# Performance work log

Hardware: AMD Instinct MI355X
Metric: run time of the kernel (lower is better)

The kernel has to match this reference:

```python
import jax, jax.numpy as jnp
import numpy as np

NUM_CLASSES = 32
SIGMA = 0.02
LOG_SIGMA = float(np.log(SIGMA))
HALF_LOG_2PI = float(0.5 * np.log(2.0 * np.pi))


def _gcn(x, adj, W1, b1, W2, b2):
    # Two-layer GCN: h = relu(A x W1 + b1); out = A h W2 + b2
    h = jax.nn.relu(jnp.einsum('bij,bjf->bif', adj, x) @ W1 + b1)
    return jnp.einsum('bij,bjf->bif', adj, h) @ W2 + b2


def setup_inputs() -> dict:
    key = jax.random.key(0)
    ks = jax.random.split(key, 10)
    B, N, F = 64, 1024, 512
    x = jax.random.normal(ks[0], (B, N, F), dtype=jnp.float32)
    adj = jax.random.uniform(ks[1], (B, N, N), dtype=jnp.float32) / N  # row-scaled dense adjacency
    masks = jax.random.randint(ks[2], (B, N, F), 0, 2, dtype=jnp.int32)
    noise = jax.random.normal(ks[3], (B, N, F), dtype=jnp.float32)
    s = 0.05
    We1 = jax.random.normal(ks[4], (F, 30), dtype=jnp.float32) * s
    be1 = jnp.zeros((30,), dtype=jnp.float32)
    We2 = jax.random.normal(ks[5], (30, 18), dtype=jnp.float32) * s
    be2 = jnp.zeros((18,), dtype=jnp.float32)
    Wd1 = jax.random.normal(ks[6], (18, 30), dtype=jnp.float32) * s
    bd1 = jnp.zeros((30,), dtype=jnp.float32)
    Wd2 = jax.random.normal(ks[7], (30, F), dtype=jnp.float32) * s
    bd2 = jnp.zeros((F,), dtype=jnp.float32)
    return dict(x=x, adj=adj, masks=masks, noise=noise, We1=We1, be1=be1,
                We2=We2, be2=be2, Wd1=Wd1, bd1=bd1, Wd2=Wd2, bd2=bd2)


def reference(x, adj, masks, noise, We1, be1, We2, be2, Wd1, bd1, Wd2, bd2):
    enc = _gcn(x, adj, We1, be1, We2, be2)            # [B,N,18]
    dec = _gcn(enc, adj, Wd1, bd1, Wd2, bd2)          # [B,N,F]
    dec_act = jnp.concatenate(
        (jax.nn.softmax(dec[..., :NUM_CLASSES], axis=-1),
         jax.nn.sigmoid(dec[..., NUM_CLASSES:])), axis=-1)
    m = masks.astype(dec_act.dtype)
    # Vectorized masked reparameterized Gaussian sample: s = mu + sigma*eps
    sampled = dec_act + m * (SIGMA * noise)
    # log N(s; mu, sigma) = -eps^2/2 - log(sigma) - 0.5*log(2pi), summed over masked entries
    lp_elem = -0.5 * noise * noise - LOG_SIGMA - HALF_LOG_2PI
    log_probs = jnp.sum(m * lp_elem, axis=(1, 2))      # [B]
    return dec, sampled, log_probs
```

## Files before the change

kernel.cpp:

```cpp
#include <hip/hip_runtime.h>

#define B_ 64
#define NN 1024
#define FF 512

typedef float  fx4 __attribute__((ext_vector_type(4)));
typedef float  fx2 __attribute__((ext_vector_type(2)));
typedef int    ix4 __attribute__((ext_vector_type(4)));
typedef unsigned int   ux4i __attribute__((ext_vector_type(4)));
typedef unsigned int   ux2i __attribute__((ext_vector_type(2)));
typedef unsigned short us4  __attribute__((ext_vector_type(4)));
typedef short  sx8 __attribute__((ext_vector_type(8)));

#define FP8_SCALE   16384.0f
#define INV_SCALE   6.103515625e-5f

static __device__ __forceinline__ unsigned short f2bf(float f){
    union { float f; unsigned u; } v; v.f = f;
    unsigned r = v.u + 0x7FFFu + ((v.u >> 16) & 1u);
    return (unsigned short)(r >> 16);
}
static __device__ __forceinline__ float bf2f(unsigned short h){
    union { unsigned u; float f; } v; v.u = ((unsigned)h) << 16;
    return v.f;
}
static __device__ __forceinline__ unsigned cvt_pk_bf16(float lo, float hi){
    unsigned r;
    asm("v_cvt_pk_bf16_f32 %0, %1, %2" : "=v"(r) : "v"(lo), "v"(hi));
    return r;
}
static __device__ __forceinline__ sx8 pack_bf16x8(fx4 v0, fx4 v1){
    union { unsigned u[4]; sx8 s; } r;
    r.u[0] = cvt_pk_bf16(v0[0], v0[1]);
    r.u[1] = cvt_pk_bf16(v0[2], v0[3]);
    r.u[2] = cvt_pk_bf16(v1[0], v1[1]);
    r.u[3] = cvt_pk_bf16(v1[2], v1[3]);
    return r.s;
}

__global__ __launch_bounds__(512) void k_xw1(
    const float* __restrict__ x, const float* __restrict__ We1,
    unsigned short* __restrict__ u1T){
    __shared__ unsigned short wls[32*512];
    int tid = threadIdx.x;
    for (int i = tid; i < 32*512; i += 512){
        int col = i >> 9, k = i & 511;
        float v = (col < 30) ? We1[k*30 + col] : 0.f;
        wls[col*512 + ((((k >> 3) ^ (col & 7)) << 3) | (k & 7))] = f2bf(v);
    }
    __syncthreads();
    int w = tid >> 6, l = tid & 63;
    int lr = l & 15, kq = l >> 4;
    int b = blockIdx.y;
    int rowb = blockIdx.x*128 + w*16;
    const float* xp = x + ((size_t)b*NN + rowb + lr)*FF + kq*8;
    fx4 acc0 = {0,0,0,0}, acc1 = {0,0,0,0};
    int c0 = lr, c1 = 16 + lr;
    #pragma unroll 4
    for (int kk = 0; kk < FF; kk += 32){
        fx4 v0 = *(const fx4*)(xp + kk);
        fx4 v1 = *(const fx4*)(xp + kk + 4);
        sx8 a = pack_bf16x8(v0, v1);
        int chunk = (kk >> 3) + kq;
        sx8 b0 = *(const sx8*)(wls + c0*512 + ((chunk ^ (c0 & 7)) << 3));
        sx8 b1 = *(const sx8*)(wls + c1*512 + ((chunk ^ (c1 & 7)) << 3));
        acc0 = __builtin_amdgcn_mfma_f32_16x16x32_bf16(a, b0, acc0, 0, 0, 0);
        acc1 = __builtin_amdgcn_mfma_f32_16x16x32_bf16(a, b1, acc1, 0, 0, 0);
    }
    int row0 = rowb + kq*4;
    us4 o0 = { f2bf(acc0[0]), f2bf(acc0[1]), f2bf(acc0[2]), f2bf(acc0[3]) };
    us4 o1 = { f2bf(acc1[0]), f2bf(acc1[1]), f2bf(acc1[2]), f2bf(acc1[3]) };
    *(us4*)(u1T + ((size_t)b*32 + c0)*NN + row0) = o0;
    *(us4*)(u1T + ((size_t)b*32 + c1)*NN + row0) = o1;
}

__global__ __launch_bounds__(256) void k_cvt_h1(
    const float* __restrict__ adjf, unsigned char* __restrict__ adj8,
    const unsigned short* __restrict__ uT, const float* __restrict__ bias,
    unsigned short* __restrict__ outT){
    __shared__ unsigned short uts[32*NN];
    int tid = threadIdx.x;
    int rt = blockIdx.x, b = blockIdx.y;
    const ux4i* src = (const ux4i*)(uT + (size_t)b*32*NN);
    #pragma unroll
    for (int i = 0; i < 16; i++){
        int j = tid + i*256;
        int c = j >> 7;
        ux4i v = src[j];
        int dst = (j*16) ^ ((c & 7) << 4);
        *(ux4i*)((char*)uts + dst) = v;
    }
    __syncthreads();
    int w = tid >> 6, l = tid & 63;
    int lr = l & 15, lk = (l >> 4) * 8;
    size_t aoff = (size_t)b*NN*NN + (size_t)(rt*128 + w*32 + lr)*NN + lk;
    int c0 = lr, c1 = 16 + lr;
    fx4 acc00 = {0,0,0,0}, acc01 = {0,0,0,0}, acc10 = {0,0,0,0}, acc11 = {0,0,0,0};
    #pragma unroll 4
    for (int kk = 0; kk < NN; kk += 32){
        fx4 v00 = *(const fx4*)(adjf + aoff + kk);
        fx4 v01 = *(const fx4*)(adjf + aoff + kk + 4);
        fx4 v10 = *(const fx4*)(adjf + aoff + 16*NN + kk);
        fx4 v11 = *(const fx4*)(adjf + aoff + 16*NN + kk + 4);
        sx8 a0 = pack_bf16x8(v00, v01);
        sx8 a1 = pack_bf16x8(v10, v11);
        {
            const float S = FP8_SCALE;
            int d0 = __builtin_amdgcn_cvt_pk_fp8_f32(v00[0]*S, v00[1]*S, 0, false);
            d0     = __builtin_amdgcn_cvt_pk_fp8_f32(v00[2]*S, v00[3]*S, d0, true);
            int d1 = __builtin_amdgcn_cvt_pk_fp8_f32(v01[0]*S, v01[1]*S, 0, false);
            d1     = __builtin_amdgcn_cvt_pk_fp8_f32(v01[2]*S, v01[3]*S, d1, true);
            ux2i s0 = { (unsigned)d0, (unsigned)d1 };
            *(ux2i*)(adj8 + aoff + kk) = s0;
            int d2 = __builtin_amdgcn_cvt_pk_fp8_f32(v10[0]*S, v10[1]*S, 0, false);
            d2     = __builtin_amdgcn_cvt_pk_fp8_f32(v10[2]*S, v10[3]*S, d2, true);
            int d3 = __builtin_amdgcn_cvt_pk_fp8_f32(v11[0]*S, v11[1]*S, 0, false);
            d3     = __builtin_amdgcn_cvt_pk_fp8_f32(v11[2]*S, v11[3]*S, d3, true);
            ux2i s1 = { (unsigned)d2, (unsigned)d3 };
            *(ux2i*)(adj8 + aoff + 16*NN + kk) = s1;
        }
        int kb = (kk + lk) * 2;
        sx8 b0 = *(const sx8*)((const char*)uts + ((c0*2048 + kb) ^ ((c0 & 7) << 4)));
        sx8 b1 = *(const sx8*)((const char*)uts + ((c1*2048 + kb) ^ ((c1 & 7) << 4)));
        acc00 = __builtin_amdgcn_mfma_f32_16x16x32_bf16(a0, b0, acc00, 0, 0, 0);
        acc01 = __builtin_amdgcn_mfma_f32_16x16x32_bf16(a0, b1, acc01, 0, 0, 0);
        acc10 = __builtin_amdgcn_mfma_f32_16x16x32_bf16(a1, b0, acc10, 0, 0, 0);
        acc11 = __builtin_amdgcn_mfma_f32_16x16x32_bf16(a1, b1, acc11, 0, 0, 0);
    }
    float bias0 = (c0 < 30) ? bias[c0] : 0.f;
    float bias1 = 0.f;
    if (c1 < 30) bias1 = bias[c1];
    int lq = l >> 4;
    #pragma unroll
    for (int mt = 0; mt < 2; mt++){
        int row0 = rt*128 + w*32 + mt*16 + lq*4;
        fx4 am0 = mt ? acc10 : acc00;
        fx4 am1 = mt ? acc11 : acc01;
        #pragma unroll
        for (int ct = 0; ct < 2; ct++){
            fx4 a = ct ? am1 : am0;
            float bb = ct ? bias1 : bias0;
            int col = ct ? c1 : c0;
            us4 o;
            #pragma unroll
            for (int j = 0; j < 4; j++){
                float v = fmaxf(a[j] + bb, 0.f);
                o[j] = f2bf(v);
            }
            *(us4*)(outT + ((size_t)b*32 + col)*NN + row0) = o;
        }
    }
}

template<int RM>
__global__ __launch_bounds__(256) void k_adjf8(
    const unsigned char* __restrict__ adj8,
    const unsigned short* __restrict__ uT,
    const float* __restrict__ bias, int biasN, float oscale,
    unsigned short* __restrict__ outT){
    __shared__ unsigned short uts[32*NN];
    int tid = threadIdx.x;
    int rt = blockIdx.x, b = blockIdx.y;
    const ux4i* src = (const ux4i*)(uT + (size_t)b*32*NN);
    #pragma unroll
    for (int i = 0; i < 16; i++){
        int j = tid + i*256;
        int c = j >> 7;
        ux4i v = src[j];
        int dst = (j*16) ^ ((c & 7) << 4);
        *(ux4i*)((char*)uts + dst) = v;
    }
    __syncthreads();
    int w = tid >> 6, l = tid & 63;
    int lr = l & 15, lk = (l >> 4) * 8;
    size_t aoff = (size_t)b*NN*NN + (size_t)(rt*128 + w*32 + lr)*NN + lk;
    int c0 = lr, c1 = 16 + lr;
    fx4 acc00 = {0,0,0,0}, acc01 = {0,0,0,0}, acc10 = {0,0,0,0}, acc11 = {0,0,0,0};
    #pragma unroll 4
    for (int kk = 0; kk < NN; kk += 32){
        ux2i q0 = *(const ux2i*)(adj8 + aoff + kk);
        ux2i q1 = *(const ux2i*)(adj8 + aoff + 16*NN + kk);
        fx2 f0 = __builtin_amdgcn_cvt_pk_f32_fp8((int)q0[0], false);
        fx2 f1 = __builtin_amdgcn_cvt_pk_f32_fp8((int)q0[0], true);
        fx2 f2 = __builtin_amdgcn_cvt_pk_f32_fp8((int)q0[1], false);
        fx2 f3 = __builtin_amdgcn_cvt_pk_f32_fp8((int)q0[1], true);
        fx2 g0 = __builtin_amdgcn_cvt_pk_f32_fp8((int)q1[0], false);
        fx2 g1 = __builtin_amdgcn_cvt_pk_f32_fp8((int)q1[0], true);
        fx2 g2 = __builtin_amdgcn_cvt_pk_f32_fp8((int)q1[1], false);
        fx2 g3 = __builtin_amdgcn_cvt_pk_f32_fp8((int)q1[1], true);
        union { unsigned u[4]; sx8 s; } A0, A1;
        A0.u[0] = cvt_pk_bf16(f0[0], f0[1]);
        A0.u[1] = cvt_pk_bf16(f1[0], f1[1]);
        A0.u[2] = cvt_pk_bf16(f2[0], f2[1]);
        A0.u[3] = cvt_pk_bf16(f3[0], f3[1]);
        A1.u[0] = cvt_pk_bf16(g0[0], g0[1]);
        A1.u[1] = cvt_pk_bf16(g1[0], g1[1]);
        A1.u[2] = cvt_pk_bf16(g2[0], g2[1]);
        A1.u[3] = cvt_pk_bf16(g3[0], g3[1]);
        int kb = (kk + lk) * 2;
        sx8 b0 = *(const sx8*)((const char*)uts + ((c0*2048 + kb) ^ ((c0 & 7) << 4)));
        sx8 b1 = *(const sx8*)((const char*)uts + ((c1*2048 + kb) ^ ((c1 & 7) << 4)));
        acc00 = __builtin_amdgcn_mfma_f32_16x16x32_bf16(A0.s, b0, acc00, 0, 0, 0);
        acc01 = __builtin_amdgcn_mfma_f32_16x16x32_bf16(A0.s, b1, acc01, 0, 0, 0);
        acc10 = __builtin_amdgcn_mfma_f32_16x16x32_bf16(A1.s, b0, acc10, 0, 0, 0);
        acc11 = __builtin_amdgcn_mfma_f32_16x16x32_bf16(A1.s, b1, acc11, 0, 0, 0);
    }
    float bias0 = 0.f, bias1 = 0.f;
    if (bias){
        if (c0 < biasN) bias0 = bias[c0];
        if (c1 < biasN) bias1 = bias[c1];
    }
    int lq = l >> 4;
    #pragma unroll
    for (int mt = 0; mt < 2; mt++){
        int row0 = rt*128 + w*32 + mt*16 + lq*4;
        fx4 am0 = mt ? acc10 : acc00;
        fx4 am1 = mt ? acc11 : acc01;
        #pragma unroll
        for (int ct = 0; ct < 2; ct++){
            fx4 a = ct ? am1 : am0;
            float bb = ct ? bias1 : bias0;
            int col = ct ? c1 : c0;
            us4 o;
            #pragma unroll
            for (int j = 0; j < 4; j++){
                float v = (a[j] + bb) * oscale;
                o[j] = f2bf(v);
            }
            if (RM){
                #pragma unroll
                for (int j = 0; j < 4; j++)
                    outT[((size_t)b*NN + row0 + j)*32 + col] = o[j];
            } else {
                *(us4*)(outT + ((size_t)b*32 + col)*NN + row0) = o;
            }
        }
    }
}

template<int JI, int CO, bool RELU>
__global__ __launch_bounds__(256) void k_tiny(
    const unsigned short* __restrict__ inT, const float* __restrict__ W,
    const float* __restrict__ bias, float oscale,
    unsigned short* __restrict__ outT){
    int n = blockIdx.x*256 + threadIdx.x;
    int b = blockIdx.y;
    const unsigned short* ip = inT + (size_t)b*32*NN + n;
    float in[JI];
    #pragma unroll
    for (int j = 0; j < JI; j++) in[j] = bf2f(ip[j*NN]);
    float acc[CO];
    #pragma unroll
    for (int c = 0; c < CO; c++) acc[c] = bias ? bias[c] : 0.f;
    #pragma unroll
    for (int j = 0; j < JI; j++){
        #pragma unroll
        for (int c = 0; c < CO; c++) acc[c] += in[j] * W[j*CO + c];
    }
    unsigned short* op = outT + (size_t)b*32*NN + n;
    #pragma unroll
    for (int c = 0; c < 32; c++){
        float v = (c < CO) ? (RELU ? fmaxf(acc[c], 0.f) : acc[c]) * oscale : 0.f;
        op[c*NN] = f2bf(v);
    }
}

__global__ __launch_bounds__(512, 4) void k_dec(
    const unsigned short* __restrict__ v2R,
    const float* __restrict__ Wd2, const float* __restrict__ bd2,
    const int* __restrict__ masks, const float* __restrict__ noise,
    float* __restrict__ dec, float* __restrict__ sampled, float* __restrict__ part){
    __shared__ unsigned short wls[512*40];
    __shared__ float dls[16][516];
    __shared__ float red[8];
    int tid = threadIdx.x;
    for (int i = tid; i < 512*32; i += 512){
        int col = i & 511, k = i >> 9;
        float v = (k < 30) ? Wd2[k*512 + col] : 0.f;
        wls[col*40 + k] = f2bf(v);
    }
    int w = tid >> 6, l = tid & 63;
    int lr = l & 15, kq = l >> 4;
    const float LPC = 2.9930844722234733f;
    float lpacc = 0.f;
    __syncthreads();
    #pragma unroll
    for (int it = 0; it < 4; it++){
        int rbase = blockIdx.x*64 + it*16;
        sx8 a = *(const sx8*)(v2R + (size_t)(rbase + lr)*32 + kq*8);
        #pragma unroll
        for (int i = 0; i < 4; i++){
            int c = (w + 8*i)*16 + lr;
            sx8 bb = *(const sx8*)(wls + c*40 + kq*8);
            fx4 acc = {0,0,0,0};
            acc = __builtin_amdgcn_mfma_f32_16x16x32_bf16(a, bb, acc, 0, 0, 0);
            float bi = bd2[c];
            #pragma unroll
            for (int j = 0; j < 4; j++)
                dls[kq*4 + j][c] = acc[j] + bi;
        }
        __syncthreads();
        #pragma unroll
        for (int s = 0; s < 2; s++){
            int rloc = w + 8*s;
            size_t off = (size_t)(rbase + rloc)*FF + l*8;
            fx4 d0 = *(const fx4*)&dls[rloc][l*8];
            fx4 d1 = *(const fx4*)&dls[rloc][l*8 + 4];
            ix4 m0 = *(const ix4*)(masks + off);
            ix4 m1 = *(const ix4*)(masks + off + 4);
            fx4 z0 = *(const fx4*)(noise + off);
            fx4 z1 = *(const fx4*)(noise + off + 4);
            float av[8];
            #pragma unroll
            for (int i = 0; i < 4; i++){
                av[i]   = 1.f/(1.f + __expf(-d0[i]));
                av[4+i] = 1.f/(1.f + __expf(-d1[i]));
            }
            if (l < 4){
                float mx = d0[0];
                #pragma unroll
                for (int i = 1; i < 4; i++) mx = fmaxf(mx, d0[i]);
                #pragma unroll
                for (int i = 0; i < 4; i++) mx = fmaxf(mx, d1[i]);
                mx = fmaxf(mx, __shfl_xor(mx, 1, 4));
                mx = fmaxf(mx, __shfl_xor(mx, 2, 4));
                float e[8], ss = 0.f;
                #pragma unroll
                for (int i = 0; i < 4; i++){ e[i] = __expf(d0[i] - mx); ss += e[i]; }
                #pragma unroll
                for (int i = 0; i < 4; i++){ e[4+i] = __expf(d1[i] - mx); ss += e[4+i]; }
                ss += __shfl_xor(ss, 1, 4);
                ss += __shfl_xor(ss, 2, 4);
                float inv = 1.f / ss;
                #pragma unroll
                for (int i = 0; i < 8; i++) av[i] = e[i]*inv;
            }
            *(fx4*)(dec + off)     = d0;
            *(fx4*)(dec + off + 4) = d1;
            fx4 sm0, sm1;
            #pragma unroll
            for (int i = 0; i < 4; i++){
                float mi0 = (float)m0[i], zi0 = z0[i];
                float mi1 = (float)m1[i], zi1 = z1[i];
                sm0[i] = av[i]   + mi0*(0.02f*zi0);
                sm1[i] = av[4+i] + mi1*(0.02f*zi1);
                lpacc = fmaf(mi0, LPC - 0.5f*zi0*zi0, lpacc);
                lpacc = fmaf(mi1, LPC - 0.5f*zi1*zi1, lpacc);
            }
            *(fx4*)(sampled + off)     = sm0;
            *(fx4*)(sampled + off + 4) = sm1;
        }
        __syncthreads();
    }
    #pragma unroll
    for (int off = 32; off > 0; off >>= 1) lpacc += __shfl_xor(lpacc, off);
    if (l == 0) red[w] = lpacc;
    __syncthreads();
    if (tid == 0){
        float s = 0.f;
        #pragma unroll
        for (int i = 0; i < 8; i++) s += red[i];
        part[blockIdx.x] = s;
    }
}

__global__ void k_lp(const float* __restrict__ part, float* __restrict__ logp){
    int t = threadIdx.x;
    float s = 0.f;
    #pragma unroll
    for (int i = 0; i < 16; i++) s += part[t*16 + i];
    logp[t] = s;
}

extern "C" void kernel_launch(void* const* d_in, const int* in_sizes, int n_in,
                              void* d_out, int out_size, void* d_ws, size_t ws_size,
                              hipStream_t stream){
    const float* x     = (const float*)d_in[0];
    const float* adj   = (const float*)d_in[1];
    const int*   masks = (const int*)  d_in[2];
    const float* noise = (const float*)d_in[3];
    const float* We1   = (const float*)d_in[4];
    const float* be1   = (const float*)d_in[5];
    const float* We2   = (const float*)d_in[6];
    const float* be2   = (const float*)d_in[7];
    const float* Wd1   = (const float*)d_in[8];
    const float* bd1   = (const float*)d_in[9];
    const float* Wd2   = (const float*)d_in[10];
    const float* bd2   = (const float*)d_in[11];

    float* dec     = (float*)d_out;
    float* sampled = dec + (size_t)B_*NN*FF;
    float* logp    = sampled + (size_t)B_*NN*FF;
    unsigned char* adj8 = (unsigned char*)d_out;
    unsigned short* bufA = (unsigned short*)d_ws;
    unsigned short* bufB = bufA + (size_t)B_*32*NN;
    float* part = (float*)bufB;

    k_xw1<<<dim3(8, B_), 512, 0, stream>>>(x, We1, bufA);
    k_cvt_h1<<<dim3(8, B_), 256, 0, stream>>>(adj, adj8, bufA, be1, bufB);
    k_tiny<30,18,false><<<dim3(4, B_), 256, 0, stream>>>(bufB, We2, nullptr, INV_SCALE, bufA);
    k_adjf8<0><<<dim3(8, B_), 256, 0, stream>>>(adj8, bufA, be2, 18, INV_SCALE, bufB);
    k_adjf8<0><<<dim3(8, B_), 256, 0, stream>>>(adj8, bufB, nullptr, 0, 1.0f, bufA);
    k_tiny<18,30,true><<<dim3(4, B_), 256, 0, stream>>>(bufA, Wd1, bd1, INV_SCALE, bufB);
    k_adjf8<1><<<dim3(8, B_), 256, 0, stream>>>(adj8, bufB, nullptr, 0, 1.0f, bufA);
    k_dec<<<1024, 512, 0, stream>>>(bufA, Wd2, bd2, masks, noise, dec, sampled, part);
    k_lp<<<1, 64, 0, stream>>>(part, logp);
}
```

Before: 350.7 us.

## Restructure decoder output kernel to keep MFMA results in registers, dropping LDS staging

The final decoder kernel now swaps the MFMA operand roles so each lane holds output columns of its own row directly in registers. This removes the shared-memory staging buffer and the per-iteration barriers. Each wave handles 16 rows across all 512 columns, and the block count is halved with k_lp adjusted to match. Global access becomes 16-byte chunks with row-strided lanes rather than contiguous 2KB rows, which may reduce coalescing on the large masks, noise, dec and sampled streams. The occupancy hint is also dropped.

Measured after the change: 370.2 us. 1.06x slower.

```diff
diff --git a/kernel.cpp b/kernel.cpp
--- a/kernel.cpp
+++ b/kernel.cpp
@@ -265,13 +265,12 @@
     }
 }
 
-__global__ __launch_bounds__(512, 4) void k_dec(
+__global__ __launch_bounds__(512) void k_dec(
     const unsigned short* __restrict__ v2R,
     const float* __restrict__ Wd2, const float* __restrict__ bd2,
     const int* __restrict__ masks, const float* __restrict__ noise,
     float* __restrict__ dec, float* __restrict__ sampled, float* __restrict__ part){
     __shared__ unsigned short wls[512*40];
-    __shared__ float dls[16][516];
     __shared__ float red[8];
     int tid = threadIdx.x;
     for (int i = tid; i < 512*32; i += 512){
@@ -279,78 +278,75 @@
         float v = (k < 30) ? Wd2[k*512 + col] : 0.f;
         wls[col*40 + k] = f2bf(v);
     }
+    __syncthreads();
     int w = tid >> 6, l = tid & 63;
     int lr = l & 15, kq = l >> 4;
+    int row = blockIdx.x*128 + w*16 + lr;
+    size_t rowoff = (size_t)row * FF;
+    sx8 bv = *(const sx8*)(v2R + (size_t)row*32 + kq*8);
+    int cb = kq*4;
     const float LPC = 2.9930844722234733f;
     float lpacc = 0.f;
-    __syncthreads();
-    #pragma unroll
-    for (int it = 0; it < 4; it++){
-        int rbase = blockIdx.x*64 + it*16;
-        sx8 a = *(const sx8*)(v2R + (size_t)(rbase + lr)*32 + kq*8);
-        #pragma unroll
-        for (int i = 0; i < 4; i++){
-            int c = (w + 8*i)*16 + lr;
-            sx8 bb = *(const sx8*)(wls + c*40 + kq*8);
-            fx4 acc = {0,0,0,0};
-            acc = __builtin_amdgcn_mfma_f32_16x16x32_bf16(a, bb, acc, 0, 0, 0);
-            float bi = bd2[c];
-            #pragma unroll
-            for (int j = 0; j < 4; j++)
-                dls[kq*4 + j][c] = acc[j] + bi;
+    fx4 dsm[2];
+    #pragma unroll
+    for (int t = 0; t < 2; t++){
+        sx8 af = *(const sx8*)(wls + (t*16 + lr)*40 + kq*8);
+        fx4 acc = {0,0,0,0};
+        acc = __builtin_amdgcn_mfma_f32_16x16x32_bf16(af, bv, acc, 0, 0, 0);
+        fx4 bi = *(const fx4*)(bd2 + t*16 + cb);
+        #pragma unroll
+        for (int j = 0; j < 4; j++) dsm[t][j] = acc[j] + bi[j];
+    }
+    float mx = dsm[0][0];
+    #pragma unroll
+    for (int j = 1; j < 4; j++) mx = fmaxf(mx, dsm[0][j]);
+    #pragma unroll
+    for (int j = 0; j < 4; j++) mx = fmaxf(mx, dsm[1][j]);
+    mx = fmaxf(mx, __shfl_xor(mx, 16));
+    mx = fmaxf(mx, __shfl_xor(mx, 32));
+    float e[8], ss = 0.f;
+    #pragma unroll
+    for (int j = 0; j < 4; j++){ e[j]   = __expf(dsm[0][j] - mx); ss += e[j]; }
+    #pragma unroll
+    for (int j = 0; j < 4; j++){ e[4+j] = __expf(dsm[1][j] - mx); ss += e[4+j]; }
+    ss += __shfl_xor(ss, 16);
+    ss += __shfl_xor(ss, 32);
+    float inv = 1.f / ss;
+    #pragma unroll
+    for (int t = 0; t < 2; t++){
+        size_t off = rowoff + t*16 + cb;
+        ix4 m = *(const ix4*)(masks + off);
+        fx4 z = *(const fx4*)(noise + off);
+        *(fx4*)(dec + off) = dsm[t];
+        fx4 sm;
+        #pragma unroll
+        for (int j = 0; j < 4; j++){
+            float mi = (float)m[j], zi = z[j];
+            sm[j] = e[t*4+j]*inv + mi*(0.02f*zi);
+            lpacc = fmaf(mi, LPC - 0.5f*zi*zi, lpacc);
         }
-        __syncthreads();
-        #pragma unroll
-        for (int s = 0; s < 2; s++){
-            int rloc = w + 8*s;
-            size_t off = (size_t)(rbase + rloc)*FF + l*8;
-            fx4 d0 = *(const fx4*)&dls[rloc][l*8];
-            fx4 d1 = *(const fx4*)&dls[rloc][l*8 + 4];
-            ix4 m0 = *(const ix4*)(masks + off);
-            ix4 m1 = *(const ix4*)(masks + off + 4);
-            fx4 z0 = *(const fx4*)(noise + off);
-            fx4 z1 = *(const fx4*)(noise + off + 4);
-            float av[8];
-            #pragma unroll
-            for (int i = 0; i < 4; i++){
-                av[i]   = 1.f/(1.f + __expf(-d0[i]));
-                av[4+i] = 1.f/(1.f + __expf(-d1[i]));
-            }
-            if (l < 4){
-                float mx = d0[0];
-                #pragma unroll
-                for (int i = 1; i < 4; i++) mx = fmaxf(mx, d0[i]);
-                #pragma unroll
-                for (int i = 0; i < 4; i++) mx = fmaxf(mx, d1[i]);
-                mx = fmaxf(mx, __shfl_xor(mx, 1, 4));
-                mx = fmaxf(mx, __shfl_xor(mx, 2, 4));
-                float e[8], ss = 0.f;
-                #pragma unroll
-                for (int i = 0; i < 4; i++){ e[i] = __expf(d0[i] - mx); ss += e[i]; }
-                #pragma unroll
-                for (int i = 0; i < 4; i++){ e[4+i] = __expf(d1[i] - mx); ss += e[4+i]; }
-                ss += __shfl_xor(ss, 1, 4);
-                ss += __shfl_xor(ss, 2, 4);
-                float inv = 1.f / ss;
-                #pragma unroll
-                for (int i = 0; i < 8; i++) av[i] = e[i]*inv;
-            }
-            *(fx4*)(dec + off)     = d0;
-            *(fx4*)(dec + off + 4) = d1;
-            fx4 sm0, sm1;
-            #pragma unroll
-            for (int i = 0; i < 4; i++){
-                float mi0 = (float)m0[i], zi0 = z0[i];
-                float mi1 = (float)m1[i], zi1 = z1[i];
-                sm0[i] = av[i]   + mi0*(0.02f*zi0);
-                sm1[i] = av[4+i] + mi1*(0.02f*zi1);
-                lpacc = fmaf(mi0, LPC - 0.5f*zi0*zi0, lpacc);
-                lpacc = fmaf(mi1, LPC - 0.5f*zi1*zi1, lpacc);
-            }
-            *(fx4*)(sampled + off)     = sm0;
-            *(fx4*)(sampled + off + 4) = sm1;
+        *(fx4*)(sampled + off) = sm;
+    }
+    #pragma unroll 4
+    for (int t = 2; t < 32; t++){
+        sx8 af = *(const sx8*)(wls + (t*16 + lr)*40 + kq*8);
+        fx4 acc = {0,0,0,0};
+        acc = __builtin_amdgcn_mfma_f32_16x16x32_bf16(af, bv, acc, 0, 0, 0);
+        fx4 bi = *(const fx4*)(bd2 + t*16 + cb);
+        size_t off = rowoff + t*16 + cb;
+        ix4 m = *(const ix4*)(masks + off);
+        fx4 z = *(const fx4*)(noise + off);
+        fx4 d, sm;
+        #pragma unroll
+        for (int j = 0; j < 4; j++){
+            d[j] = acc[j] + bi[j];
+            float av = 1.f / (1.f + __expf(-d[j]));
+            float mi = (float)m[j], zi = z[j];
+            sm[j] = av + mi*(0.02f*zi);
+            lpacc = fmaf(mi, LPC - 0.5f*zi*zi, lpacc);
         }
-        __syncthreads();
+        *(fx4*)(dec + off) = d;
+        *(fx4*)(sampled + off) = sm;
     }
     #pragma unroll
     for (int off = 32; off > 0; off >>= 1) lpacc += __shfl_xor(lpacc, off);
@@ -368,7 +364,7 @@
     int t = threadIdx.x;
     float s = 0.f;
     #pragma unroll
-    for (int i = 0; i < 16; i++) s += part[t*16 + i];
+    for (int i = 0; i < 8; i++) s += part[t*8 + i];
     logp[t] = s;
 }
 
@@ -403,6 +399,6 @@
     k_adjf8<0><<<dim3(8, B_), 256, 0, stream>>>(adj8, bufB, nullptr, 0, 1.0f, bufA);
     k_tiny<18,30,true><<<dim3(4, B_), 256, 0, stream>>>(bufA, Wd1, bd1, INV_SCALE, bufB);
     k_adjf8<1><<<dim3(8, B_), 256, 0, stream>>>(adj8, bufB, nullptr, 0, 1.0f, bufA);
-    k_dec<<<1024, 512, 0, stream>>>(bufA, Wd2, bd2, masks, noise, dec, sampled, part);
+    k_dec<<<512, 512, 0, stream>>>(bufA, Wd2, bd2, masks, noise, dec, sampled, part);
     k_lp<<<1, 64, 0, stream>>>(part, logp);
 }
```
